# Performance work log

Hardware: AMD Instinct MI355X
Metric: run time of the kernel (lower is better)

## Reference

```python
import jax, jax.numpy as jnp
import numpy as np

IN_F = 256
OUT_F = 256
H = 4
DH = OUT_F // H  # 64
N = 6144


def setup_inputs() -> dict:
    key = jax.random.key(0)
    ks = jax.random.split(key, 6)
    x = jax.random.normal(ks[0], (N, IN_F), dtype=jnp.float32)
    adj = jax.random.randint(ks[1], (N, N), 0, 2, dtype=jnp.int32)
    # per-head Linear(in_features, d_head): weights [H, IN_F, DH], bias [H, DH]
    W = jax.random.normal(ks[2], (H, IN_F, DH), dtype=jnp.float32) / np.sqrt(IN_F)
    Wb = jax.random.normal(ks[3], (H, DH), dtype=jnp.float32) * 0.01
    # per-head Linear(2*d_head, 1): weights [H, 2*DH], bias [H]
    A = jax.random.normal(ks[4], (H, 2 * DH), dtype=jnp.float32) / np.sqrt(2 * DH)
    Ab = jax.random.normal(ks[5], (H,), dtype=jnp.float32) * 0.01
    return {"x": x, "adj": adj, "W": W, "Wb": Wb, "A": A, "Ab": Ab}


def reference(x, adj, W, Wb, A, Ab):
    # h[h,n,d] = per-head linear projection of node features
    h = jnp.einsum("ni,hid->hnd", x, W) + Wb[:, None, :]
    a_src, a_dst = A[:, :DH], A[:, DH:]
    # score(i,j) = a_src . h_i + a_dst . h_j + b  (decomposed concat-linear)
    s_src = jnp.einsum("hnd,hd->hn", h, a_src) + Ab[:, None]  # [H, N]
    s_dst = jnp.einsum("hnd,hd->hn", h, a_dst)                # [H, N]
    scores = s_src[:, :, None] + s_dst[:, None, :]            # [H, N, N]
    # Faithful to source: non-edges get score 0.0 (not -inf) before softmax
    scores = jnp.where(adj[None, :, :] > 0, scores, 0.0)
    probs = jax.nn.softmax(scores, axis=-1)                   # row softmax
    out = jnp.einsum("hij,hjd->hid", probs, h)                # [H, N, DH]
    # concat heads along feature dim -> [N, H*DH]
    return jnp.transpose(out, (1, 0, 2)).reshape(N, H * DH)
```

## Files before the change

kernel.cpp:

```cpp
#include <hip/hip_runtime.h>
#include <stdint.h>

#define NN 6144
#define NC 576

typedef float f32x4 __attribute__((ext_vector_type(4)));
typedef __bf16 bf16x8v __attribute__((ext_vector_type(8)));

__device__ __forceinline__ unsigned short f2bf(float f) {
  unsigned u = __float_as_uint(f);
  u += 0x7FFFu + ((u >> 16) & 1u);
  return (unsigned short)(u >> 16);
}

__device__ __forceinline__ float bf2f(unsigned short s) {
  unsigned u = (unsigned)s << 16;
  return __uint_as_float(u);
}

__device__ __forceinline__ unsigned char f2e4m3(float f) {
  unsigned u = __float_as_uint(f);
  unsigned sgn = (u >> 24) & 0x80u;
  unsigned au = u & 0x7FFFFFFFu;
  if (au >= 0x43E00000u) return (unsigned char)(sgn | 0x7E);
  if (au < 0x3C800000u) {
    int q = (int)rintf(__uint_as_float(au) * 512.0f);
    return (unsigned char)(sgn | (q >= 8 ? 0x08 : q));
  }
  unsigned r = au + 0x7FFFFu + ((au >> 20) & 1u);
  int e = (int)(r >> 23) - 127;
  unsigned m = (r >> 20) & 7u;
  return (unsigned char)(sgn | ((unsigned)(e + 7) << 3) | m);
}

__device__ __forceinline__ unsigned short pack2(float a, float b) {
  return (unsigned short)f2e4m3(a) | ((unsigned short)f2e4m3(b) << 8);
}

__device__ __forceinline__ void async_load16(const void* g, void* l) {
  __builtin_amdgcn_global_load_lds(
      (__attribute__((address_space(1))) void*)(uintptr_t)g,
      (__attribute__((address_space(3))) void*)(uint32_t)(uintptr_t)l,
      16, 0, 0);
}

__global__ __launch_bounds__(256) void p0s(
    const float* __restrict__ x, const float* __restrict__ W,
    const float* __restrict__ Aw, const float* __restrict__ Wb,
    unsigned short* __restrict__ xsw, unsigned short* __restrict__ wsw,
    float* __restrict__ Acat, float* __restrict__ T)
{
  const int bid = blockIdx.x, t = threadIdx.x;
  if (bid < 8) {
#pragma unroll
    for (int i = 0; i < 4; ++i) {
      const int e = bid * 256 + t + i * 2048;
      const int l = e & 63, kc = (e >> 6) & 7, ct = e >> 9;
      const int c = ct * 16 + (l & 15);
      const int h = c >> 6, d0 = c & 63;
      const int ks = kc * 32 + (l >> 4) * 8;
      const float* src = W + h * 16384 + ks * 64 + d0;
      unsigned uu[4];
#pragma unroll
      for (int j = 0; j < 4; ++j)
        uu[j] = (unsigned)f2bf(src[(2*j) * 64]) | ((unsigned)f2bf(src[(2*j+1) * 64]) << 16);
      *(uint4*)(wsw + (size_t)e * 8) = (uint4){uu[0], uu[1], uu[2], uu[3]};
    }
    return;
  }
  if (bid == 8) {
    T[t] = 0.f;
    const int h = t >> 6, d = t & 63;
    Acat[t]       = Aw[h * 128 + d];
    Acat[256 + t] = Aw[h * 128 + 64 + d];
    Acat[512 + t] = Wb[t];
    return;
  }
  const int tid = (bid - 9) * 256 + t;
#pragma unroll 4
  for (int i = 0; i < 32; ++i) {
    const int e = tid + i * 6144;
    const int l = e & 63, kc = (e >> 6) & 7, mt = e >> 9;
    const int node = mt * 16 + (l & 15);
    const int ks = kc * 32 + (l >> 4) * 8;
    const float4* xp = (const float4*)(x + (size_t)node * 256 + ks);
    float4 v0 = xp[0], v1 = xp[1];
    uint4 o;
    o.x = (unsigned)f2bf(v0.x) | ((unsigned)f2bf(v0.y) << 16);
    o.y = (unsigned)f2bf(v0.z) | ((unsigned)f2bf(v0.w) << 16);
    o.z = (unsigned)f2bf(v1.x) | ((unsigned)f2bf(v1.y) << 16);
    o.w = (unsigned)f2bf(v1.z) | ((unsigned)f2bf(v1.w) << 16);
    *(uint4*)(xsw + (size_t)e * 8) = o;
  }
}

__global__ __launch_bounds__(256) void k1m(
    const unsigned short* __restrict__ xsw, const unsigned short* __restrict__ wsw,
    const float* __restrict__ Acat, const float* __restrict__ Ab,
    const int* __restrict__ adj, unsigned char* __restrict__ A8,
    unsigned char* __restrict__ V8, float* __restrict__ e_src, float* __restrict__ T)
{
  __shared__ unsigned char lv[4][4096];
  __shared__ float lt[256];
  const int t = threadIdx.x;

  if (blockIdx.x >= 192) {
    const int pb = blockIdx.x - 192;
    const int4* a4 = (const int4*)adj;
    unsigned* o1 = (unsigned*)A8;
    const int g0 = pb * 2048 + t;
    int4 q[8];
#pragma unroll
    for (int j = 0; j < 8; ++j) q[j] = a4[g0 + j * 256];
#pragma unroll
    for (int j = 0; j < 8; ++j)
      o1[g0 + j * 256] = (unsigned)q[j].x * 0x38u | (unsigned)q[j].y * 0x3800u |
                         (unsigned)q[j].z * 0x380000u | (unsigned)q[j].w * 0x38000000u;
    return;
  }

  const int w = t >> 6, l = t & 63;
  const int v = blockIdx.x * 4 + w;
  const int mt = v >> 1, nh = v & 1;
  const int i0 = mt * 16, c0 = nh * 128;
  const int lm = l & 15, lk = l >> 4;

  lt[t] = 0.f;
  __syncthreads();

  f32x4 acc[8];
#pragma unroll
  for (int nt = 0; nt < 8; ++nt) acc[nt] = (f32x4){0.f, 0.f, 0.f, 0.f};

  const unsigned short* ap = xsw + ((size_t)mt * 512 + l) * 8;
  const unsigned short* bp = wsw + ((size_t)nh * 4096 + l) * 8;

#pragma unroll
  for (int kc = 0; kc < 8; ++kc) {
    bf16x8v a = *(const bf16x8v*)(ap + (size_t)kc * 512);
#pragma unroll
    for (int nt = 0; nt < 8; ++nt) {
      bf16x8v b = *(const bf16x8v*)(bp + ((size_t)nt * 512 + kc * 64) * 8);
      acc[nt] = __builtin_amdgcn_mfma_f32_16x16x32_bf16(a, b, acc[nt], 0, 0, 0);
    }
  }

  float asv[8], adv[8];
#pragma unroll
  for (int nt = 0; nt < 8; ++nt) {
    const int cc = c0 + nt * 16 + lm;
    const float wb = Acat[512 + cc];
#pragma unroll
    for (int rr = 0; rr < 4; ++rr) acc[nt][rr] += wb;
    asv[nt] = Acat[cc];
    adv[nt] = Acat[256 + cc];
  }

#pragma unroll
  for (int nt = 0; nt < 8; ++nt)
    atomicAdd(&lt[c0 + nt * 16 + lm], acc[nt][0] + acc[nt][1] + acc[nt][2] + acc[nt][3]);

  float ss[2][4], sd[2][4];
#pragma unroll
  for (int hl = 0; hl < 2; ++hl)
#pragma unroll
    for (int rr = 0; rr < 4; ++rr) {
      float s1 = 0.f, s2 = 0.f;
#pragma unroll
      for (int j = 0; j < 4; ++j) {
        s1 += acc[hl * 4 + j][rr] * asv[hl * 4 + j];
        s2 += acc[hl * 4 + j][rr] * adv[hl * 4 + j];
      }
      ss[hl][rr] = s1; sd[hl][rr] = s2;
    }
#pragma unroll
  for (int off = 1; off < 16; off <<= 1)
#pragma unroll
    for (int hl = 0; hl < 2; ++hl)
#pragma unroll
      for (int rr = 0; rr < 4; ++rr) {
        ss[hl][rr] += __shfl_xor(ss[hl][rr], off);
        sd[hl][rr] += __shfl_xor(sd[hl][rr], off);
      }

  float ed[2][4];
#pragma unroll
  for (int hl = 0; hl < 2; ++hl)
#pragma unroll
    for (int rr = 0; rr < 4; ++rr) ed[hl][rr] = expf(sd[hl][rr]);

  if (lm == 0) {
#pragma unroll
    for (int hl = 0; hl < 2; ++hl) {
      const int hh = nh * 2 + hl;
      const float ab = Ab[hh];
#pragma unroll
      for (int rr = 0; rr < 4; ++rr)
        e_src[(size_t)hh * NN + i0 + lk * 4 + rr] = expf(ss[hl][rr] + ab);
    }
  }

  unsigned char* mylv = lv[w];
#pragma unroll
  for (int nt = 0; nt < 8; ++nt) {
    const int hl = nt >> 2;
    const int d = (nt & 3) * 16 + lm;
    const int lcE = hl * 128 + d;
    const int lcP = lcE + 64;
    *(unsigned short*)(mylv + lcE * 16 + lk * 4)     = pack2(ed[hl][0] * acc[nt][0], ed[hl][1] * acc[nt][1]);
    *(unsigned short*)(mylv + lcE * 16 + lk * 4 + 2) = pack2(ed[hl][2] * acc[nt][2], ed[hl][3] * acc[nt][3]);
    *(unsigned short*)(mylv + lcP * 16 + lk * 4)     = pack2(acc[nt][0], acc[nt][1]);
    *(unsigned short*)(mylv + lcP * 16 + lk * 4 + 2) = pack2(acc[nt][2], acc[nt][3]);
  }
#pragma unroll
  for (int j = 0; j < 4; ++j) {
    const int lc = j * 64 + l;
    uint4 val = *(const uint4*)(mylv + lc * 16);
    *(uint4*)(V8 + (size_t)(nh * 256 + lc) * NN + i0) = val;
  }
  if (lm == 0) {
#pragma unroll
    for (int hl = 0; hl < 2; ++hl) {
      const int hh = nh * 2 + hl;
      unsigned char* pq = V8 + (size_t)(512 + hh) * NN + i0 + lk * 4;
      *(unsigned short*)pq       = pack2(ed[hl][0], ed[hl][1]);
      *(unsigned short*)(pq + 2) = pack2(ed[hl][2], ed[hl][3]);
    }
    if (nh == 0)
      *(unsigned*)(V8 + (size_t)516 * NN + i0 + lk * 4) = 0x38383838u;
  }

  __syncthreads();
  atomicAdd(&T[t], lt[t]);
}

__global__ __launch_bounds__(256, 3) void k2_gemm(
    const unsigned char* __restrict__ A8, const unsigned char* __restrict__ V8,
    unsigned short* __restrict__ out2b, float* __restrict__ out2e, int nks)
{
  __shared__ unsigned char lB[144 * 128];
  const int t   = threadIdx.x;
  const int cb  = blockIdx.x & 3;
  const int rb  = (blockIdx.x >> 2) & 31;
  const int ks  = blockIdx.x >> 7;
  const int krange = NN / nks;
  const int i0 = rb * 192, n0 = cb * 144, k0 = ks * krange;
  const int w = t >> 6, l = t & 63;
  const int lm = l & 15, lk = l >> 4;

  f32x4 acc[3][9];
#pragma unroll
  for (int mt = 0; mt < 3; ++mt)
#pragma unroll
    for (int nt = 0; nt < 9; ++nt) acc[mt][nt] = (f32x4){0.f, 0.f, 0.f, 0.f};

  int scol[5], sgr[5];
#pragma unroll
  for (int u = 0; u < 5; ++u) {
    const int gi = u * 256 + t;
    scol[u] = gi >> 3;
    sgr[u]  = (gi & 7) ^ (scol[u] & 7);
  }
  const int dbase4 = (1024 + (t & ~63)) * 16;

  const unsigned char* gA0 = A8 + (size_t)(i0 + w * 48 + lm) * NN + k0 + lk * 32;
  const unsigned char* gBb = V8 + (size_t)n0 * NN + k0;

  const int iters = krange / 128;
  for (int it = 0; it < iters; ++it) {
    const unsigned char* gB = gBb + it * 128;
#pragma unroll
    for (int u = 0; u < 4; ++u)
      async_load16(gB + (size_t)scol[u] * NN + sgr[u] * 16,
                   (char*)lB + (size_t)(u * 256 + (t & ~63)) * 16);
    if (t < 128)
      async_load16(gB + (size_t)scol[4] * NN + sgr[4] * 16, (char*)lB + dbase4);
    longlong2 afr[3][2];
    const unsigned char* gA = gA0 + it * 128;
#pragma unroll
    for (int mt = 0; mt < 3; ++mt) {
      afr[mt][0] = *(const longlong2*)(gA + (size_t)mt * 16 * NN);
      afr[mt][1] = *(const longlong2*)(gA + (size_t)mt * 16 * NN + 16);
    }
    __syncthreads();
#pragma unroll
    for (int b = 0; b < 2; ++b) {
#pragma unroll
      for (int nt = 0; nt < 9; ++nt) {
        const int cc = nt * 16 + lm;
        const int pos = (lk * 2 + b) ^ (cc & 7);
        longlong2 bv = *(const longlong2*)(lB + cc * 128 + pos * 16);
#pragma unroll
        for (int mt = 0; mt < 3; ++mt) {
          acc[mt][nt] = __builtin_amdgcn_mfma_f32_16x16x32_fp8_fp8(
              afr[mt][b].x, bv.x, acc[mt][nt], 0, 0, 0);
          acc[mt][nt] = __builtin_amdgcn_mfma_f32_16x16x32_fp8_fp8(
              afr[mt][b].y, bv.y, acc[mt][nt], 0, 0, 0);
        }
      }
    }
    __syncthreads();
  }

  unsigned short* lw = (unsigned short*)(lB + w * 4608);
  float* oe = out2e + (size_t)ks * ((size_t)NN * 64);
  unsigned short* pb = out2b + ((size_t)(ks * 4 + cb) * NN + i0 + w * 48) * 144;
#pragma unroll
  for (int mt = 0; mt < 3; ++mt) {
#pragma unroll
    for (int nt = 0; nt < 9; ++nt) {
      const int coll = nt * 16 + lm;
#pragma unroll
      for (int rr = 0; rr < 4; ++rr)
        lw[(lk * 4 + rr) * 144 + coll] = f2bf(acc[mt][nt][rr]);
      if (cb == 3 && nt >= 5) {
        const int row = i0 + w * 48 + mt * 16 + lk * 4;
#pragma unroll
        for (int rr = 0; rr < 4; ++rr)
          oe[(size_t)(row + rr) * 64 + (n0 + coll - 512)] = acc[mt][nt][rr];
      }
    }
    const uint4* ls = (const uint4*)(lB + w * 4608);
    char* dst = (char*)(pb + (size_t)mt * 16 * 144);
    for (int s = l; s < 288; s += 64)
      *(uint4*)(dst + s * 16) = ls[s];
  }
}

__global__ __launch_bounds__(256) void k3_final(
    const unsigned short* __restrict__ out2b, const float* __restrict__ out2e,
    const float* __restrict__ e_src, const float* __restrict__ T,
    float* __restrict__ out, int nks)
{
  const int n = blockIdx.x, c = threadIdx.x;
  const int h = c >> 6, d = c & 63;
  const int cS = h * 128 + d, cP = cS + 64;
  const int cbS = cS / 144, ofS = cS % 144;
  const int cbP = cP / 144, ofP = cP % 144;
  float Se = 0.f, Sp = 0.f, E = 0.f, dg = 0.f;
  for (int s = 0; s < nks; ++s) {
    const unsigned short* base = out2b + (size_t)s * 4 * NN * 144;
    Se += bf2f(base[((size_t)cbS * NN + n) * 144 + ofS]);
    Sp += bf2f(base[((size_t)cbP * NN + n) * 144 + ofP]);
    const float* re = out2e + (size_t)s * NN * 64 + (size_t)n * 64;
    E  += re[h];
    dg += re[4];
  }
  float e = e_src[h * NN + n];
  float D = e * E + ((float)NN - dg);
  out[(size_t)n * 256 + c] = (e * Se + (T[c] - Sp)) / D;
}

extern "C" void kernel_launch(void* const* d_in, const int* in_sizes, int n_in,
                              void* d_out, int out_size, void* d_ws, size_t ws_size,
                              hipStream_t stream) {
  const float* x  = (const float*)d_in[0];
  const int*   adj= (const int*)d_in[1];
  const float* W  = (const float*)d_in[2];
  const float* Wb = (const float*)d_in[3];
  const float* Aw = (const float*)d_in[4];
  const float* Ab = (const float*)d_in[5];
  float* out = (float*)d_out;
  char* ws = (char*)d_ws;
  unsigned char* V8 = (unsigned char*)ws;
  float* e_src = (float*)(ws + 3538944);
  float* T     = (float*)(ws + 3637248);
  float* Acat  = (float*)(ws + 3638272);
  unsigned short* wsw = (unsigned short*)(ws + 3641344);
  unsigned short* xsw = (unsigned short*)(ws + 3772416);
  unsigned char* A8   = (unsigned char*)(ws + 6918144);
  unsigned short* out2b = (unsigned short*)(ws + 44666880);
  float* out2e = (float*)(ws + 87134208);

  const size_t slabB = (size_t)4 * NN * 144 * 2;
  const size_t slabE = (size_t)NN * 64 * 4;
  int nks = 2;
  if (ws_size >= 87134208 + 6 * slabE)                    nks = 6;
  else if (ws_size >= 44666880 + 4 * slabB + 4 * slabE)   nks = 4;

  hipLaunchKernelGGL(p0s, dim3(33), dim3(256), 0, stream,
                     x, W, Aw, Wb, xsw, wsw, Acat, T);
  hipLaunchKernelGGL(k1m, dim3(4800), dim3(256), 0, stream,
                     xsw, wsw, Acat, Ab, adj, A8, V8, e_src, T);
  hipLaunchKernelGGL(k2_gemm, dim3(128 * nks), dim3(256), 0, stream, A8, V8, out2b, out2e, nks);
  hipLaunchKernelGGL(k3_final, dim3(NN), dim3(256), 0, stream, out2b, out2e, e_src, T, out, nks);
}
```

Measured before the change: 300.1 us.

## Fuse adjacency int32-to-fp8 conversion into GEMM A-operand loads

Result: slower. 336.0 us (+12.0%).

```diff
diff --git a/kernel.cpp b/kernel.cpp
--- a/kernel.cpp
+++ b/kernel.cpp
@@ -77,9 +77,9 @@
     return;
   }
   const int tid = (bid - 9) * 256 + t;
-#pragma unroll 4
-  for (int i = 0; i < 32; ++i) {
-    const int e = tid + i * 6144;
+#pragma unroll
+  for (int i = 0; i < 4; ++i) {
+    const int e = tid + i * 49152;
     const int l = e & 63, kc = (e >> 6) & 7, mt = e >> 9;
     const int node = mt * 16 + (l & 15);
     const int ks = kc * 32 + (l >> 4) * 8;
@@ -97,27 +97,11 @@
 __global__ __launch_bounds__(256) void k1m(
     const unsigned short* __restrict__ xsw, const unsigned short* __restrict__ wsw,
     const float* __restrict__ Acat, const float* __restrict__ Ab,
-    const int* __restrict__ adj, unsigned char* __restrict__ A8,
     unsigned char* __restrict__ V8, float* __restrict__ e_src, float* __restrict__ T)
 {
   __shared__ unsigned char lv[4][4096];
   __shared__ float lt[256];
   const int t = threadIdx.x;
-
-  if (blockIdx.x >= 192) {
-    const int pb = blockIdx.x - 192;
-    const int4* a4 = (const int4*)adj;
-    unsigned* o1 = (unsigned*)A8;
-    const int g0 = pb * 2048 + t;
-    int4 q[8];
-#pragma unroll
-    for (int j = 0; j < 8; ++j) q[j] = a4[g0 + j * 256];
-#pragma unroll
-    for (int j = 0; j < 8; ++j)
-      o1[g0 + j * 256] = (unsigned)q[j].x * 0x38u | (unsigned)q[j].y * 0x3800u |
-                         (unsigned)q[j].z * 0x380000u | (unsigned)q[j].w * 0x38000000u;
-    return;
-  }
 
   const int w = t >> 6, l = t & 63;
   const int v = blockIdx.x * 4 + w;
@@ -235,14 +219,16 @@
 }
 
 __global__ __launch_bounds__(256, 3) void k2_gemm(
-    const unsigned char* __restrict__ A8, const unsigned char* __restrict__ V8,
+    const int* __restrict__ adj, const unsigned char* __restrict__ V8,
     unsigned short* __restrict__ out2b, float* __restrict__ out2e, int nks)
 {
   __shared__ unsigned char lB[144 * 128];
   const int t   = threadIdx.x;
-  const int cb  = blockIdx.x & 3;
-  const int rb  = (blockIdx.x >> 2) & 31;
-  const int ks  = blockIdx.x >> 7;
+  const int bid = blockIdx.x;
+  const int ks  = bid >> 7;
+  const int r   = bid & 127;
+  const int cb  = (r >> 3) & 3;
+  const int rb  = (r & 7) | ((r >> 5) << 3);
   const int krange = NN / nks;
   const int i0 = rb * 192, n0 = cb * 144, k0 = ks * krange;
   const int w = t >> 6, l = t & 63;
@@ -263,7 +249,7 @@
   }
   const int dbase4 = (1024 + (t & ~63)) * 16;
 
-  const unsigned char* gA0 = A8 + (size_t)(i0 + w * 48 + lm) * NN + k0 + lk * 32;
+  const int* gA0 = adj + (size_t)(i0 + w * 48 + lm) * NN + k0 + lk * 32;
   const unsigned char* gBb = V8 + (size_t)n0 * NN + k0;
 
   const int iters = krange / 128;
@@ -275,12 +261,24 @@
                    (char*)lB + (size_t)(u * 256 + (t & ~63)) * 16);
     if (t < 128)
       async_load16(gB + (size_t)scol[4] * NN + sgr[4] * 16, (char*)lB + dbase4);
+
     longlong2 afr[3][2];
-    const unsigned char* gA = gA0 + it * 128;
+    const int* gA = gA0 + it * 128;
 #pragma unroll
     for (int mt = 0; mt < 3; ++mt) {
-      afr[mt][0] = *(const longlong2*)(gA + (size_t)mt * 16 * NN);
-      afr[mt][1] = *(const longlong2*)(gA + (size_t)mt * 16 * NN + 16);
+      const int4* p = (const int4*)(gA + (size_t)mt * 16 * NN);
+#pragma unroll
+      for (int hb = 0; hb < 2; ++hb) {
+        int4 q0 = p[hb * 4 + 0], q1 = p[hb * 4 + 1];
+        int4 q2 = p[hb * 4 + 2], q3 = p[hb * 4 + 3];
+        unsigned u0 = (unsigned)(q0.x | (q0.y << 8) | (q0.z << 16) | (q0.w << 24)) * 0x38u;
+        unsigned u1 = (unsigned)(q1.x | (q1.y << 8) | (q1.z << 16) | (q1.w << 24)) * 0x38u;
+        unsigned u2 = (unsigned)(q2.x | (q2.y << 8) | (q2.z << 16) | (q2.w << 24)) * 0x38u;
+        unsigned u3 = (unsigned)(q3.x | (q3.y << 8) | (q3.z << 16) | (q3.w << 24)) * 0x38u;
+        afr[mt][hb].x = (long long)(((unsigned long long)u1 << 32) | u0);
+        afr[mt][hb].y = (long long)(((unsigned long long)u3 << 32) | u2);
+        __builtin_amdgcn_sched_barrier(0);
+      }
     }
     __syncthreads();
 #pragma unroll
@@ -368,7 +366,6 @@
   float* Acat  = (float*)(ws + 3638272);
   unsigned short* wsw = (unsigned short*)(ws + 3641344);
   unsigned short* xsw = (unsigned short*)(ws + 3772416);
-  unsigned char* A8   = (unsigned char*)(ws + 6918144);
   unsigned short* out2b = (unsigned short*)(ws + 44666880);
   float* out2e = (float*)(ws + 87134208);
 
@@ -378,10 +375,10 @@
   if (ws_size >= 87134208 + 6 * slabE)                    nks = 6;
   else if (ws_size >= 44666880 + 4 * slabB + 4 * slabE)   nks = 4;
 
-  hipLaunchKernelGGL(p0s, dim3(33), dim3(256), 0, stream,
+  hipLaunchKernelGGL(p0s, dim3(201), dim3(256), 0, stream,
                      x, W, Aw, Wb, xsw, wsw, Acat, T);
-  hipLaunchKernelGGL(k1m, dim3(4800), dim3(256), 0, stream,
-                     xsw, wsw, Acat, Ab, adj, A8, V8, e_src, T);
-  hipLaunchKernelGGL(k2_gemm, dim3(128 * nks), dim3(256), 0, stream, A8, V8, out2b, out2e, nks);
+  hipLaunchKernelGGL(k1m, dim3(192), dim3(256), 0, stream,
+                     xsw, wsw, Acat, Ab, V8, e_src, T);
+  hipLaunchKernelGGL(k2_gemm, dim3(128 * nks), dim3(256), 0, stream, adj, V8, out2b, out2e, nks);
   hipLaunchKernelGGL(k3_final, dim3(NN), dim3(256), 0, stream, out2b, out2e, e_src, T, out, nks);
 }
```

## Pack adjacency into a bitmask and expand to fp8 inside the GEMM

Applied to the files above, without the earlier changes.

Result: faster. 277.9 us (-7.4%).

```diff
diff --git a/kernel.cpp b/kernel.cpp
--- a/kernel.cpp
+++ b/kernel.cpp
@@ -77,9 +77,9 @@
     return;
   }
   const int tid = (bid - 9) * 256 + t;
-#pragma unroll 4
-  for (int i = 0; i < 32; ++i) {
-    const int e = tid + i * 6144;
+#pragma unroll
+  for (int i = 0; i < 4; ++i) {
+    const int e = tid + i * 49152;
     const int l = e & 63, kc = (e >> 6) & 7, mt = e >> 9;
     const int node = mt * 16 + (l & 15);
     const int ks = kc * 32 + (l >> 4) * 8;
@@ -97,7 +97,7 @@
 __global__ __launch_bounds__(256) void k1m(
     const unsigned short* __restrict__ xsw, const unsigned short* __restrict__ wsw,
     const float* __restrict__ Acat, const float* __restrict__ Ab,
-    const int* __restrict__ adj, unsigned char* __restrict__ A8,
+    const int* __restrict__ adj, unsigned* __restrict__ bm,
     unsigned char* __restrict__ V8, float* __restrict__ e_src, float* __restrict__ T)
 {
   __shared__ unsigned char lv[4][4096];
@@ -106,16 +106,19 @@
 
   if (blockIdx.x >= 192) {
     const int pb = blockIdx.x - 192;
-    const int4* a4 = (const int4*)adj;
-    unsigned* o1 = (unsigned*)A8;
-    const int g0 = pb * 2048 + t;
+    const int tid = pb * 256 + t;
+    const int4* src = (const int4*)adj + (size_t)tid * 8;
     int4 q[8];
 #pragma unroll
-    for (int j = 0; j < 8; ++j) q[j] = a4[g0 + j * 256];
-#pragma unroll
-    for (int j = 0; j < 8; ++j)
-      o1[g0 + j * 256] = (unsigned)q[j].x * 0x38u | (unsigned)q[j].y * 0x3800u |
-                         (unsigned)q[j].z * 0x380000u | (unsigned)q[j].w * 0x38000000u;
+    for (int j = 0; j < 8; ++j) q[j] = src[j];
+    unsigned b = 0;
+#pragma unroll
+    for (int j = 0; j < 8; ++j) {
+      unsigned nib = (unsigned)q[j].x | ((unsigned)q[j].y << 1) |
+                     ((unsigned)q[j].z << 2) | ((unsigned)q[j].w << 3);
+      b |= nib << (4 * j);
+    }
+    bm[tid] = b;
     return;
   }
 
@@ -235,7 +238,7 @@
 }
 
 __global__ __launch_bounds__(256, 3) void k2_gemm(
-    const unsigned char* __restrict__ A8, const unsigned char* __restrict__ V8,
+    const unsigned* __restrict__ bm, const unsigned char* __restrict__ V8,
     unsigned short* __restrict__ out2b, float* __restrict__ out2e, int nks)
 {
   __shared__ unsigned char lB[144 * 128];
@@ -263,7 +266,7 @@
   }
   const int dbase4 = (1024 + (t & ~63)) * 16;
 
-  const unsigned char* gA0 = A8 + (size_t)(i0 + w * 48 + lm) * NN + k0 + lk * 32;
+  const unsigned* gA0 = bm + (size_t)(i0 + w * 48 + lm) * (NN / 32) + (k0 >> 5) + lk;
   const unsigned char* gBb = V8 + (size_t)n0 * NN + k0;
 
   const int iters = krange / 128;
@@ -275,12 +278,25 @@
                    (char*)lB + (size_t)(u * 256 + (t & ~63)) * 16);
     if (t < 128)
       async_load16(gB + (size_t)scol[4] * NN + sgr[4] * 16, (char*)lB + dbase4);
+
+    unsigned bits[3];
+#pragma unroll
+    for (int mt = 0; mt < 3; ++mt)
+      bits[mt] = gA0[(size_t)mt * 16 * (NN / 32) + it * 4];
+
     longlong2 afr[3][2];
-    const unsigned char* gA = gA0 + it * 128;
 #pragma unroll
     for (int mt = 0; mt < 3; ++mt) {
-      afr[mt][0] = *(const longlong2*)(gA + (size_t)mt * 16 * NN);
-      afr[mt][1] = *(const longlong2*)(gA + (size_t)mt * 16 * NN + 16);
+      unsigned u[8];
+#pragma unroll
+      for (int i = 0; i < 8; ++i) {
+        unsigned nib = (bits[mt] >> (4 * i)) & 0xFu;
+        u[i] = ((nib * 0x00204081u) & 0x01010101u) << 3;
+      }
+      afr[mt][0].x = (long long)(((unsigned long long)u[1] << 32) | u[0]);
+      afr[mt][0].y = (long long)(((unsigned long long)u[3] << 32) | u[2]);
+      afr[mt][1].x = (long long)(((unsigned long long)u[5] << 32) | u[4]);
+      afr[mt][1].y = (long long)(((unsigned long long)u[7] << 32) | u[6]);
     }
     __syncthreads();
 #pragma unroll
@@ -312,12 +328,12 @@
       const int coll = nt * 16 + lm;
 #pragma unroll
       for (int rr = 0; rr < 4; ++rr)
-        lw[(lk * 4 + rr) * 144 + coll] = f2bf(acc[mt][nt][rr]);
+        lw[(lk * 4 + rr) * 144 + coll] = f2bf(acc[mt][nt][rr] * 64.0f);
       if (cb == 3 && nt >= 5) {
         const int row = i0 + w * 48 + mt * 16 + lk * 4;
 #pragma unroll
         for (int rr = 0; rr < 4; ++rr)
-          oe[(size_t)(row + rr) * 64 + (n0 + coll - 512)] = acc[mt][nt][rr];
+          oe[(size_t)(row + rr) * 64 + (n0 + coll - 512)] = acc[mt][nt][rr] * 64.0f;
       }
     }
     const uint4* ls = (const uint4*)(lB + w * 4608);
@@ -368,7 +384,7 @@
   float* Acat  = (float*)(ws + 3638272);
   unsigned short* wsw = (unsigned short*)(ws + 3641344);
   unsigned short* xsw = (unsigned short*)(ws + 3772416);
-  unsigned char* A8   = (unsigned char*)(ws + 6918144);
+  unsigned* bm = (unsigned*)(ws + 6918144);
   unsigned short* out2b = (unsigned short*)(ws + 44666880);
   float* out2e = (float*)(ws + 87134208);
 
@@ -378,10 +394,10 @@
   if (ws_size >= 87134208 + 6 * slabE)                    nks = 6;
   else if (ws_size >= 44666880 + 4 * slabB + 4 * slabE)   nks = 4;
 
-  hipLaunchKernelGGL(p0s, dim3(33), dim3(256), 0, stream,
+  hipLaunchKernelGGL(p0s, dim3(201), dim3(256), 0, stream,
                      x, W, Aw, Wb, xsw, wsw, Acat, T);
   hipLaunchKernelGGL(k1m, dim3(4800), dim3(256), 0, stream,
-                     xsw, wsw, Acat, Ab, adj, A8, V8, e_src, T);
-  hipLaunchKernelGGL(k2_gemm, dim3(128 * nks), dim3(256), 0, stream, A8, V8, out2b, out2e, nks);
+                     xsw, wsw, Acat, Ab, adj, bm, V8, e_src, T);
+  hipLaunchKernelGGL(k2_gemm, dim3(128 * nks), dim3(256), 0, stream, bm, V8, out2b, out2e, nks);
   hipLaunchKernelGGL(k3_final, dim3(NN), dim3(256), 0, stream, out2b, out2e, e_src, T, out, nks);
 }
```
